# Kernel optimization log

Measured on AMD Instinct MI355X. Metric: run time of the kernel, lower is better.

## Reference

```python
import jax, jax.numpy as jnp
import numpy as np

B, N, K = 4, 4096, 2
C_IN, H, C_OUT = 32, 64, 32
BN_EPS = 1e-5
GIN_EPS = 0.0  # non-trainable buffer, default 0


def setup_inputs() -> dict:
    key = jax.random.key(0)
    ks = jax.random.split(key, 32)
    d = {}
    d["x"] = jax.random.normal(ks[0], (B, N, K, C_IN), jnp.float32)
    # dense binary adjacency, avg degree ~32
    d["adj"] = (jax.random.uniform(ks[1], (B, N, N)) < (32.0 / N)).astype(jnp.float32)
    d["mask"] = jax.random.uniform(ks[2], (B, N)) < 0.9
    dims = [(C_IN, H, H), (H, H, H), (H, H, C_OUT)]
    i = 3
    for l, (ci, h, co) in enumerate(dims):
        d[f"Wa{l}"] = jax.random.normal(ks[i], (ci, h), jnp.float32) / np.sqrt(ci).astype(np.float32); i += 1
        d[f"ba{l}"] = jnp.zeros((h,), jnp.float32)
        d[f"bng{l}"] = jnp.ones((h,), jnp.float32)
        d[f"bnb{l}"] = jnp.zeros((h,), jnp.float32)
        d[f"bnm{l}"] = jax.random.normal(ks[i], (h,), jnp.float32) * 0.1; i += 1
        d[f"bnv{l}"] = jax.random.uniform(ks[i], (h,), jnp.float32) * 0.5 + 0.5; i += 1
        d[f"Wb{l}"] = jax.random.normal(ks[i], (h, co), jnp.float32) / np.sqrt(h).astype(np.float32); i += 1
        d[f"bb{l}"] = jnp.zeros((co,), jnp.float32)
    for l in range(2):  # outer BatchNorm1d(hidden) before layers 1 and 2
        d[f"og{l}"] = jnp.ones((H,), jnp.float32)
        d[f"ob{l}"] = jnp.zeros((H,), jnp.float32)
        d[f"om{l}"] = jax.random.normal(ks[i], (H,), jnp.float32) * 0.1; i += 1
        d[f"ov{l}"] = jax.random.uniform(ks[i], (H,), jnp.float32) * 0.5 + 0.5; i += 1
    return d


def _bn(h, g, b, m, v):
    # eval-mode BatchNorm1d: per-channel affine with running stats
    return (h - m) * jax.lax.rsqrt(v + BN_EPS) * g + b


def _forward(x, adj, mask, p):
    m4 = mask[:, :, None, None]
    for l in range(3):
        if l > 0:
            # outer BN applied only at masked nodes (unmasked stay zero)
            xn = _bn(x, p[f"og{l-1}"], p[f"ob{l-1}"], p[f"om{l-1}"], p[f"ov{l-1}"])
            x = jnp.where(m4, xn, 0.0)
        Bx, Nx, Kx, Cx = x.shape
        xf = x.reshape(Bx, Nx, Kx * Cx)
        # GIN aggregation: (1+eps)*x + A @ x  (dense adj matmul)
        agg = (jnp.matmul(adj, xf) + (1.0 + GIN_EPS) * xf).reshape(Bx, Nx, Kx, Cx)
        # update MLP (lin -> relu -> BN -> lin), pointwise per node => apply to all, zero unmasked
        h = jax.nn.relu(agg @ p[f"Wa{l}"] + p[f"ba{l}"])
        h = _bn(h, p[f"bng{l}"], p[f"bnb{l}"], p[f"bnm{l}"], p[f"bnv{l}"])
        h = h @ p[f"Wb{l}"] + p[f"bb{l}"]
        x = jnp.where(m4, h, 0.0)  # scatter back into zeros at masked nodes
    return x


def reference(x, adj, mask,
              Wa0, ba0, bng0, bnb0, bnm0, bnv0, Wb0, bb0,
              Wa1, ba1, bng1, bnb1, bnm1, bnv1, Wb1, bb1,
              Wa2, ba2, bng2, bnb2, bnm2, bnv2, Wb2, bb2,
              og0, ob0, om0, ov0, og1, ob1, om1, ov1):
    p = {k: v for k, v in locals().items() if k not in ("x", "adj", "mask")}
    return _forward(x, adj, mask, p)
```

## Files before the change

### kernel.cpp

```cpp
#include <hip/hip_runtime.h>
#include <cstdint>

#define NB 4
#define NN 4096
#define CAP 128
#define BN_ROWS (NB*NN)
#define EPS_C 1e-5f

typedef __attribute__((ext_vector_type(4))) float f32x4;

__device__ inline unsigned rne16(float f) {
    unsigned u = __builtin_bit_cast(unsigned, f);
    return (u + 0x7fffu + ((u >> 16) & 1u)) >> 16;
}
__device__ inline uint32_t pack2(float a, float b) {
    return (rne16(a) & 0xffffu) | (rne16(b) << 16);
}
__device__ inline float lo2f(uint32_t u) { return __builtin_bit_cast(float, u << 16); }
__device__ inline float hi2f(uint32_t u) { return __builtin_bit_cast(float, u & 0xffff0000u); }

__global__ __launch_bounds__(256) void detect_mask_fmt(const uint8_t* __restrict__ m,
                                                       int* __restrict__ flag) {
    __shared__ int cnt;
    if (threadIdx.x == 0) cnt = 0;
    __syncthreads();
    int c = 0;
    #pragma unroll
    for (int t = 0; t < 16; t++) c += (m[threadIdx.x * 16 + t] != 0) ? 1 : 0;
    atomicAdd(&cnt, c);
    __syncthreads();
    if (threadIdx.x == 0) *flag = (cnt < 1400) ? 0 : ((cnt < 2765) ? 2 : 1);
}

__global__ __launch_bounds__(256) void convert_x(const float* __restrict__ x,
                                                 uint32_t* __restrict__ xbf) {
    int i = blockIdx.x * 256 + threadIdx.x;
    int node = i >> 5, j = i & 31;
    float f0 = x[node * 64 + j];
    float f1 = x[node * 64 + 32 + j];
    xbf[i] = pack2(f0, f1);
}

__global__ __launch_bounds__(256) void build_adj(const float* __restrict__ adj,
                                                 const void* __restrict__ mraw,
                                                 const int* __restrict__ flag,
                                                 uint16_t* __restrict__ nbr,
                                                 int* __restrict__ counts,
                                                 float* __restrict__ maskf) {
    int r = blockIdx.x;
    const int gbase = r & ~(NN - 1);
    const float4* row = (const float4*)(adj + (size_t)r * NN);
    __shared__ int cnt;
    if (threadIdx.x == 0) {
        cnt = 0;
        int f = *flag; bool v;
        if (f == 0)      v = ((const int*)mraw)[r] != 0;
        else if (f == 1) v = ((const uint8_t*)mraw)[r] != 0;
        else             v = ((const float*)mraw)[r] != 0.0f;
        maskf[r] = v ? 1.0f : 0.0f;
    }
    __syncthreads();
    uint16_t* out = nbr + (size_t)r * CAP;
    #pragma unroll
    for (int t = 0; t < 4; t++) {
        int j4 = t * 256 + threadIdx.x;
        float4 f = row[j4];
        if (f.x != 0.0f) { int p = atomicAdd(&cnt, 1); if (p < CAP) out[p] = (uint16_t)(gbase + j4 * 4 + 0); }
        if (f.y != 0.0f) { int p = atomicAdd(&cnt, 1); if (p < CAP) out[p] = (uint16_t)(gbase + j4 * 4 + 1); }
        if (f.z != 0.0f) { int p = atomicAdd(&cnt, 1); if (p < CAP) out[p] = (uint16_t)(gbase + j4 * 4 + 2); }
        if (f.w != 0.0f) { int p = atomicAdd(&cnt, 1); if (p < CAP) out[p] = (uint16_t)(gbase + j4 * 4 + 3); }
    }
    __syncthreads();
    if (threadIdx.x == 0) counts[r] = min(cnt, (int)CAP);
}

template<int CI, int CO, bool FOLD>
__global__ __launch_bounds__(256) void gin_layer_v5(
    const uint32_t* __restrict__ xin, void* __restrict__ xout,
    const uint16_t* __restrict__ nbr, const int* __restrict__ counts,
    const float* __restrict__ maskf,
    const float* __restrict__ Wa, const float* __restrict__ ba,
    const float* __restrict__ bng, const float* __restrict__ bnb,
    const float* __restrict__ bnm, const float* __restrict__ bnv,
    const float* __restrict__ Wb, const float* __restrict__ bb,
    const float* __restrict__ og, const float* __restrict__ ob,
    const float* __restrict__ om, const float* __restrict__ ov)
{
    __shared__ float aggS[4][128];
    __shared__ float hS[4][128];
    const int tid = threadIdx.x, lane = tid & 63;
    const int wvu = __builtin_amdgcn_readfirstlane(tid >> 6);
    const int node = blockIdx.x * 4 + wvu;
    const int jdx = (CI == 64) ? lane : (lane & 31);

    const int cnt = counts[node];
    const uint32_t* nbu = (const uint32_t*)(nbr + (size_t)node * CAP);
    uint32_t u = xin[(size_t)node * CI + jdx];
    float ax = lo2f(u), ay = hi2f(u);
    int j = 0;

#define GCHUNK(NCH)                                                         \
    {                                                                       \
        uint32_t t[NCH];                                                    \
        _Pragma("unroll")                                                   \
        for (int q = 0; q < NCH; q += 2) {                                  \
            uint32_t pr = nbu[(j + q) >> 1];              \
            t[q]     = xin[(size_t)(pr & 0xffffu) * CI + jdx];              \
            t[q + 1] = xin[(size_t)(pr >> 16)     * CI + jdx];              \
        }                                                                   \
        _Pragma("unroll")                                                   \
        for (int q = 0; q < NCH; q++) { ax += lo2f(t[q]); ay += hi2f(t[q]); } \
        j += NCH;                                                           \
    }

    while (j + 16 <= cnt) GCHUNK(16)
    if (j + 8 <= cnt)     GCHUNK(8)
    if (j + 4 <= cnt)     GCHUNK(4)
    if (j + 2 <= cnt)     GCHUNK(2)
    if (j < cnt) {
        uint32_t pr = nbu[j >> 1];
        uint32_t v = xin[(size_t)(pr & 0xffffu) * CI + jdx];
        ax += lo2f(v); ay += hi2f(v);
    }
#undef GCHUNK

    if (CI == 64 || lane < 32) {
        aggS[wvu][jdx]      = ax;
        aggS[wvu][CI + jdx] = ay;
    }

    const float ba_v = ba[lane];
    const float bsc  = bng[lane] * rsqrtf(bnv[lane] + EPS_C);
    const float bsh  = bnb[lane] - bnm[lane] * bsc;
    const int   co   = (CO == 64) ? lane : (lane & 31);
    float c1 = 1.0f, c0 = bb[co];
    if (FOLD) { c1 = og[co] * rsqrtf(ov[co] + EPS_C); c0 = bb[co] * c1 + ob[co] - om[co] * c1; }
    const float m = maskf[node];

    float wa[CI];
    #pragma unroll
    for (int c = 0; c < CI; c++) wa[c] = Wa[c * 64 + lane];

    float h0a = ba_v, h0b = 0.0f, h1a = ba_v, h1b = 0.0f;
    #pragma unroll
    for (int c4 = 0; c4 < CI / 4; c4++) {
        f32x4 b0 = *(const f32x4*)&aggS[wvu][c4 * 4];
        f32x4 b1 = *(const f32x4*)&aggS[wvu][CI + c4 * 4];
        h0a += b0[0] * wa[c4 * 4 + 0]; h0b += b0[1] * wa[c4 * 4 + 1];
        h0a += b0[2] * wa[c4 * 4 + 2]; h0b += b0[3] * wa[c4 * 4 + 3];
        h1a += b1[0] * wa[c4 * 4 + 0]; h1b += b1[1] * wa[c4 * 4 + 1];
        h1a += b1[2] * wa[c4 * 4 + 2]; h1b += b1[3] * wa[c4 * 4 + 3];
    }
    float h0 = fmaxf(h0a + h0b, 0.0f) * bsc + bsh;
    float h1 = fmaxf(h1a + h1b, 0.0f) * bsc + bsh;
    hS[wvu][lane]      = h0;
    hS[wvu][64 + lane] = h1;

    float wb[64];
    #pragma unroll
    for (int j2 = 0; j2 < 64; j2++) wb[j2] = Wb[j2 * CO + co];

    if (CO == 64) {
        float o0a = 0.0f, o0b = 0.0f, o1a = 0.0f, o1b = 0.0f;
        #pragma unroll
        for (int j4 = 0; j4 < 16; j4++) {
            f32x4 u0 = *(const f32x4*)&hS[wvu][j4 * 4];
            f32x4 u1 = *(const f32x4*)&hS[wvu][64 + j4 * 4];
            o0a += u0[0] * wb[j4 * 4 + 0]; o0b += u0[1] * wb[j4 * 4 + 1];
            o0a += u0[2] * wb[j4 * 4 + 2]; o0b += u0[3] * wb[j4 * 4 + 3];
            o1a += u1[0] * wb[j4 * 4 + 0]; o1b += u1[1] * wb[j4 * 4 + 1];
            o1a += u1[2] * wb[j4 * 4 + 2]; o1b += u1[3] * wb[j4 * 4 + 3];
        }
        float o0 = ((o0a + o0b) * c1 + c0) * m;
        float o1 = ((o1a + o1b) * c1 + c0) * m;
        ((uint32_t*)xout)[(size_t)node * 64 + lane] = pack2(o0, o1);
    } else {
        const int k = lane >> 5;
        float oa = 0.0f, ob_ = 0.0f;
        #pragma unroll
        for (int j4 = 0; j4 < 16; j4++) {
            f32x4 uu = *(const f32x4*)&hS[wvu][k * 64 + j4 * 4];
            oa  += uu[0] * wb[j4 * 4 + 0]; ob_ += uu[1] * wb[j4 * 4 + 1];
            oa  += uu[2] * wb[j4 * 4 + 2]; ob_ += uu[3] * wb[j4 * 4 + 3];
        }
        float o = ((oa + ob_) * c1 + c0) * m;
        ((float*)xout)[(size_t)node * 64 + lane] = o;
    }
}

extern "C" void kernel_launch(void* const* d_in, const int* in_sizes, int n_in,
                              void* d_out, int out_size, void* d_ws, size_t ws_size,
                              hipStream_t stream) {
    const float* x   = (const float*)d_in[0];
    const float* adj = (const float*)d_in[1];
    const void*  msk = d_in[2];
    const float* P[35];
    for (int i = 0; i < n_in && i < 35; i++) P[i] = (const float*)d_in[i];

    uint8_t* w = (uint8_t*)d_ws;
    size_t off = 0;
    auto take = [&](size_t bytes) -> uint8_t* {
        uint8_t* p = w + off;
        off = (off + bytes + 255) & ~(size_t)255;
        return p;
    };
    int*      flag   = (int*)     take(4);
    float*    maskf  = (float*)   take((size_t)BN_ROWS * 4);
    int*      counts = (int*)     take((size_t)BN_ROWS * 4);
    uint16_t* nbrs   = (uint16_t*)take((size_t)BN_ROWS * CAP * 2);
    uint32_t* x0bf   = (uint32_t*)take((size_t)BN_ROWS * 32 * 4);
    uint32_t* xA     = (uint32_t*)take((size_t)BN_ROWS * 64 * 4);
    uint32_t* xB     = (uint32_t*)take((size_t)BN_ROWS * 64 * 4);
    (void)ws_size; (void)in_sizes; (void)out_size;

    hipLaunchKernelGGL(detect_mask_fmt, dim3(1), dim3(256), 0, stream,
                       (const uint8_t*)msk, flag);
    hipLaunchKernelGGL(convert_x, dim3(BN_ROWS * 32 / 256), dim3(256), 0, stream,
                       x, x0bf);
    hipLaunchKernelGGL(build_adj, dim3(BN_ROWS), dim3(256), 0, stream,
                       adj, msk, flag, nbrs, counts, maskf);

    hipLaunchKernelGGL((gin_layer_v5<32, 64, true>), dim3(BN_ROWS / 4), dim3(256), 0, stream,
                       x0bf, xA, nbrs, counts, maskf,
                       P[3], P[4], P[5], P[6], P[7], P[8], P[9], P[10],
                       P[27], P[28], P[29], P[30]);
    hipLaunchKernelGGL((gin_layer_v5<64, 64, true>), dim3(BN_ROWS / 4), dim3(256), 0, stream,
                       xA, xB, nbrs, counts, maskf,
                       P[11], P[12], P[13], P[14], P[15], P[16], P[17], P[18],
                       P[31], P[32], P[33], P[34]);
    hipLaunchKernelGGL((gin_layer_v5<64, 32, false>), dim3(BN_ROWS / 4), dim3(256), 0, stream,
                       xB, (float*)d_out, nbrs, counts, maskf,
                       P[19], P[20], P[21], P[22], P[23], P[24], P[25], P[26],
                       P[27], P[28], P[29], P[30]);
}
```

Before: 507.1 us.

## Process four nodes per wavefront to amortize MLP weight loads across nodes

Each wavefront now handles four consecutive nodes instead of one, and the grid shrinks by a factor of four. Wa and Wb are loaded into registers once and reused for the four nodes' MLP steps, which cuts the redundant per-node weight traffic. The gather loop also gains a 32-wide chunk for more loads in flight. In exchange the kernel needs more LDS and has fewer blocks to spread across CUs, and the gather for the four nodes runs one after another, which may lower latency hiding.

```diff
diff --git a/kernel.cpp b/kernel.cpp
--- a/kernel.cpp
+++ b/kernel.cpp
@@ -75,7 +75,7 @@
 }
 
 template<int CI, int CO, bool FOLD>
-__global__ __launch_bounds__(256) void gin_layer_v5(
+__global__ __launch_bounds__(256) void gin_layer_v6(
     const uint32_t* __restrict__ xin, void* __restrict__ xout,
     const uint16_t* __restrict__ nbr, const int* __restrict__ counts,
     const float* __restrict__ maskf,
@@ -86,18 +86,20 @@
     const float* __restrict__ og, const float* __restrict__ ob,
     const float* __restrict__ om, const float* __restrict__ ov)
 {
-    __shared__ float aggS[4][128];
-    __shared__ float hS[4][128];
+    __shared__ float aggS[4][4][128];
+    __shared__ float hS[4][4][128];
     const int tid = threadIdx.x, lane = tid & 63;
     const int wvu = __builtin_amdgcn_readfirstlane(tid >> 6);
-    const int node = blockIdx.x * 4 + wvu;
+    const int node0 = (blockIdx.x * 4 + wvu) * 4;
     const int jdx = (CI == 64) ? lane : (lane & 31);
 
-    const int cnt = counts[node];
-    const uint32_t* nbu = (const uint32_t*)(nbr + (size_t)node * CAP);
-    uint32_t u = xin[(size_t)node * CI + jdx];
-    float ax = lo2f(u), ay = hi2f(u);
-    int j = 0;
+    for (int n = 0; n < 4; n++) {
+        const int node = node0 + n;
+        const int cnt = counts[node];
+        const uint32_t* nbu = (const uint32_t*)(nbr + (size_t)node * CAP);
+        uint32_t u = xin[(size_t)node * CI + jdx];
+        float ax = lo2f(u), ay = hi2f(u);
+        int j = 0;
 
 #define GCHUNK(NCH)                                                         \
     {                                                                       \
@@ -113,20 +115,22 @@
         j += NCH;                                                           \
     }
 
-    while (j + 16 <= cnt) GCHUNK(16)
-    if (j + 8 <= cnt)     GCHUNK(8)
-    if (j + 4 <= cnt)     GCHUNK(4)
-    if (j + 2 <= cnt)     GCHUNK(2)
-    if (j < cnt) {
-        uint32_t pr = nbu[j >> 1];
-        uint32_t v = xin[(size_t)(pr & 0xffffu) * CI + jdx];
-        ax += lo2f(v); ay += hi2f(v);
-    }
+        while (j + 32 <= cnt) GCHUNK(32)
+        if (j + 16 <= cnt)    GCHUNK(16)
+        if (j + 8 <= cnt)     GCHUNK(8)
+        if (j + 4 <= cnt)     GCHUNK(4)
+        if (j + 2 <= cnt)     GCHUNK(2)
+        if (j < cnt) {
+            uint32_t pr = nbu[j >> 1];
+            uint32_t v = xin[(size_t)(pr & 0xffffu) * CI + jdx];
+            ax += lo2f(v); ay += hi2f(v);
+        }
 #undef GCHUNK
 
-    if (CI == 64 || lane < 32) {
-        aggS[wvu][jdx]      = ax;
-        aggS[wvu][CI + jdx] = ay;
+        if (CI == 64 || lane < 32) {
+            aggS[wvu][n][jdx]      = ax;
+            aggS[wvu][n][CI + jdx] = ay;
+        }
     }
 
     const float ba_v = ba[lane];
@@ -135,56 +139,65 @@
     const int   co   = (CO == 64) ? lane : (lane & 31);
     float c1 = 1.0f, c0 = bb[co];
     if (FOLD) { c1 = og[co] * rsqrtf(ov[co] + EPS_C); c0 = bb[co] * c1 + ob[co] - om[co] * c1; }
-    const float m = maskf[node];
-
-    float wa[CI];
-    #pragma unroll
-    for (int c = 0; c < CI; c++) wa[c] = Wa[c * 64 + lane];
-
-    float h0a = ba_v, h0b = 0.0f, h1a = ba_v, h1b = 0.0f;
-    #pragma unroll
-    for (int c4 = 0; c4 < CI / 4; c4++) {
-        f32x4 b0 = *(const f32x4*)&aggS[wvu][c4 * 4];
-        f32x4 b1 = *(const f32x4*)&aggS[wvu][CI + c4 * 4];
-        h0a += b0[0] * wa[c4 * 4 + 0]; h0b += b0[1] * wa[c4 * 4 + 1];
-        h0a += b0[2] * wa[c4 * 4 + 2]; h0b += b0[3] * wa[c4 * 4 + 3];
-        h1a += b1[0] * wa[c4 * 4 + 0]; h1b += b1[1] * wa[c4 * 4 + 1];
-        h1a += b1[2] * wa[c4 * 4 + 2]; h1b += b1[3] * wa[c4 * 4 + 3];
-    }
-    float h0 = fmaxf(h0a + h0b, 0.0f) * bsc + bsh;
-    float h1 = fmaxf(h1a + h1b, 0.0f) * bsc + bsh;
-    hS[wvu][lane]      = h0;
-    hS[wvu][64 + lane] = h1;
-
-    float wb[64];
-    #pragma unroll
-    for (int j2 = 0; j2 < 64; j2++) wb[j2] = Wb[j2 * CO + co];
-
-    if (CO == 64) {
-        float o0a = 0.0f, o0b = 0.0f, o1a = 0.0f, o1b = 0.0f;
+
+    {
+        float wa[CI];
         #pragma unroll
-        for (int j4 = 0; j4 < 16; j4++) {
-            f32x4 u0 = *(const f32x4*)&hS[wvu][j4 * 4];
-            f32x4 u1 = *(const f32x4*)&hS[wvu][64 + j4 * 4];
-            o0a += u0[0] * wb[j4 * 4 + 0]; o0b += u0[1] * wb[j4 * 4 + 1];
-            o0a += u0[2] * wb[j4 * 4 + 2]; o0b += u0[3] * wb[j4 * 4 + 3];
-            o1a += u1[0] * wb[j4 * 4 + 0]; o1b += u1[1] * wb[j4 * 4 + 1];
-            o1a += u1[2] * wb[j4 * 4 + 2]; o1b += u1[3] * wb[j4 * 4 + 3];
-        }
-        float o0 = ((o0a + o0b) * c1 + c0) * m;
-        float o1 = ((o1a + o1b) * c1 + c0) * m;
-        ((uint32_t*)xout)[(size_t)node * 64 + lane] = pack2(o0, o1);
-    } else {
-        const int k = lane >> 5;
-        float oa = 0.0f, ob_ = 0.0f;
+        for (int c = 0; c < CI; c++) wa[c] = Wa[c * 64 + lane];
+
+        for (int n = 0; n < 4; n++) {
+            float h0a = ba_v, h0b = 0.0f, h1a = ba_v, h1b = 0.0f;
+            #pragma unroll
+            for (int c4 = 0; c4 < CI / 4; c4++) {
+                f32x4 b0 = *(const f32x4*)&aggS[wvu][n][c4 * 4];
+                f32x4 b1 = *(const f32x4*)&aggS[wvu][n][CI + c4 * 4];
+                h0a += b0[0] * wa[c4 * 4 + 0]; h0b += b0[1] * wa[c4 * 4 + 1];
+                h0a += b0[2] * wa[c4 * 4 + 2]; h0b += b0[3] * wa[c4 * 4 + 3];
+                h1a += b1[0] * wa[c4 * 4 + 0]; h1b += b1[1] * wa[c4 * 4 + 1];
+                h1a += b1[2] * wa[c4 * 4 + 2]; h1b += b1[3] * wa[c4 * 4 + 3];
+            }
+            float h0 = fmaxf(h0a + h0b, 0.0f) * bsc + bsh;
+            float h1 = fmaxf(h1a + h1b, 0.0f) * bsc + bsh;
+            hS[wvu][n][lane]      = h0;
+            hS[wvu][n][64 + lane] = h1;
+        }
+    }
+
+    {
+        float wb[64];
         #pragma unroll
-        for (int j4 = 0; j4 < 16; j4++) {
-            f32x4 uu = *(const f32x4*)&hS[wvu][k * 64 + j4 * 4];
-            oa  += uu[0] * wb[j4 * 4 + 0]; ob_ += uu[1] * wb[j4 * 4 + 1];
-            oa  += uu[2] * wb[j4 * 4 + 2]; ob_ += uu[3] * wb[j4 * 4 + 3];
-        }
-        float o = ((oa + ob_) * c1 + c0) * m;
-        ((float*)xout)[(size_t)node * 64 + lane] = o;
+        for (int j2 = 0; j2 < 64; j2++) wb[j2] = Wb[j2 * CO + co];
+
+        for (int n = 0; n < 4; n++) {
+            const int node = node0 + n;
+            const float m = maskf[node];
+            if (CO == 64) {
+                float o0a = 0.0f, o0b = 0.0f, o1a = 0.0f, o1b = 0.0f;
+                #pragma unroll
+                for (int j4 = 0; j4 < 16; j4++) {
+                    f32x4 u0 = *(const f32x4*)&hS[wvu][n][j4 * 4];
+                    f32x4 u1 = *(const f32x4*)&hS[wvu][n][64 + j4 * 4];
+                    o0a += u0[0] * wb[j4 * 4 + 0]; o0b += u0[1] * wb[j4 * 4 + 1];
+                    o0a += u0[2] * wb[j4 * 4 + 2]; o0b += u0[3] * wb[j4 * 4 + 3];
+                    o1a += u1[0] * wb[j4 * 4 + 0]; o1b += u1[1] * wb[j4 * 4 + 1];
+                    o1a += u1[2] * wb[j4 * 4 + 2]; o1b += u1[3] * wb[j4 * 4 + 3];
+                }
+                float o0 = ((o0a + o0b) * c1 + c0) * m;
+                float o1 = ((o1a + o1b) * c1 + c0) * m;
+                ((uint32_t*)xout)[(size_t)node * 64 + lane] = pack2(o0, o1);
+            } else {
+                const int k = lane >> 5;
+                float oa = 0.0f, ob_ = 0.0f;
+                #pragma unroll
+                for (int j4 = 0; j4 < 16; j4++) {
+                    f32x4 uu = *(const f32x4*)&hS[wvu][n][k * 64 + j4 * 4];
+                    oa  += uu[0] * wb[j4 * 4 + 0]; ob_ += uu[1] * wb[j4 * 4 + 1];
+                    oa  += uu[2] * wb[j4 * 4 + 2]; ob_ += uu[3] * wb[j4 * 4 + 3];
+                }
+                float o = ((oa + ob_) * c1 + c0) * m;
+                ((float*)xout)[(size_t)node * 64 + lane] = o;
+            }
+        }
     }
 }
 
@@ -220,15 +233,17 @@
     hipLaunchKernelGGL(build_adj, dim3(BN_ROWS), dim3(256), 0, stream,
                        adj, msk, flag, nbrs, counts, maskf);
 
-    hipLaunchKernelGGL((gin_layer_v5<32, 64, true>), dim3(BN_ROWS / 4), dim3(256), 0, stream,
+    const int LBLK = BN_ROWS / 16;
+
+    hipLaunchKernelGGL((gin_layer_v6<32, 64, true>), dim3(LBLK), dim3(256), 0, stream,
                        x0bf, xA, nbrs, counts, maskf,
                        P[3], P[4], P[5], P[6], P[7], P[8], P[9], P[10],
                        P[27], P[28], P[29], P[30]);
-    hipLaunchKernelGGL((gin_layer_v5<64, 64, true>), dim3(BN_ROWS / 4), dim3(256), 0, stream,
+    hipLaunchKernelGGL((gin_layer_v6<64, 64, true>), dim3(LBLK), dim3(256), 0, stream,
                        xA, xB, nbrs, counts, maskf,
                        P[11], P[12], P[13], P[14], P[15], P[16], P[17], P[18],
                        P[31], P[32], P[33], P[34]);
-    hipLaunchKernelGGL((gin_layer_v5<64, 32, false>), dim3(BN_ROWS / 4), dim3(256), 0, stream,
+    hipLaunchKernelGGL((gin_layer_v6<64, 32, false>), dim3(LBLK), dim3(256), 0, stream,
                        xB, (float*)d_out, nbrs, counts, maskf,
                        P[19], P[20], P[21], P[22], P[23], P[24], P[25], P[26],
                        P[27], P[28], P[29], P[30]);
```

After: 490.7 us. 1.03x faster.
